# Kernel optimization log

Hardware: AMD Instinct MI355X
Metric: run time of the kernel (lower is better)

Reference implementation:

```python
import jax, jax.numpy as jnp
import numpy as np

BATCH, SEQ, D_MODEL, STATE_DIM = 8, 2048, 1024, 1024


def setup_inputs() -> dict:
    key = jax.random.key(0)
    k1, k2, k3, k4 = jax.random.split(key, 4)
    u = jax.random.normal(k1, (BATCH, SEQ, D_MODEL), dtype=jnp.float32)
    a_params = jax.random.normal(k2, (STATE_DIM // 2,), dtype=jnp.float32) * 0.1
    # nn.Linear default init ~ U(-1/sqrt(fan_in), 1/sqrt(fan_in)); scaled normal is fine for a baseline
    B_w = jax.random.normal(k3, (STATE_DIM, D_MODEL), dtype=jnp.float32) / np.sqrt(D_MODEL).astype(np.float32)
    C_w = jax.random.normal(k4, (D_MODEL, STATE_DIM), dtype=jnp.float32) / np.sqrt(STATE_DIM).astype(np.float32)
    D = jnp.zeros((D_MODEL,), dtype=jnp.float32)
    return {"u": u, "a_params": a_params, "B_w": B_w, "C_w": C_w, "D": D}


def _cayley_circulant_eigenvalues(a_params, n):
    # Build skew-circulant first column: a[0]=0, a[1:n/2]=a_params[:n/2-1], a[n/2]=0,
    # a[n/2+1:] = -flip(a_params[:n/2-1]); eigenvalues are purely imaginary: i*omega.
    half_n = n // 2
    a_full = jnp.zeros((n,), dtype=a_params.dtype)
    a_full = a_full.at[1:half_n].set(a_params[: half_n - 1])
    a_full = a_full.at[half_n + 1 :].set(-a_params[: half_n - 1][::-1])
    omega = jnp.fft.fft(a_full).imag
    # Cayley transform (1 - i*w)/(1 + i*w) = ((1-w^2) - 2iw) / (1+w^2)
    w2 = omega * omega
    denom = 1.0 + w2
    return (((1.0 - w2) / denom) + 1j * (-2.0 * omega / denom)).astype(jnp.complex64)


def reference(u, a_params, B_w, C_w, D):
    n = B_w.shape[0]
    lambdas = _cayley_circulant_eigenvalues(a_params, n)  # (n,) complex64
    Bu = jnp.einsum("bsd,nd->bsn", u, B_w)  # (b, s, n)

    def step(h, bu_t):
        # W h via FFT diagonalization of the circulant W (W real => real part exact)
        Wh = jnp.fft.ifft(lambdas * jnp.fft.fft(h.astype(jnp.float32))).real.astype(h.dtype)
        h_new = Wh + bu_t
        return h_new, h_new

    h0 = jnp.zeros((u.shape[0], n), dtype=u.dtype)
    _, hs = jax.lax.scan(step, h0, jnp.swapaxes(Bu, 0, 1))  # hs: (s, b, n)
    y = jnp.einsum("sbn,dn->bsd", hs, C_w) + D * u  # (b, s, d)
    return y
```

## Files before the change

### kernel.cpp

```cpp
#include <hip/hip_runtime.h>
#include <math.h>

#define BATCH   8
#define SEQLEN  2048
#define DMODEL  1024
#define KFREQ   513
#define NSPEC   1024
#define NPAIR   512
#define BT_ROWS (BATCH*SEQLEN)
#define NC      32
#define TC      64

static_assert(NC * TC == SEQLEN, "chunking must cover SEQLEN");

typedef __attribute__((ext_vector_type(4))) float f32x4;
typedef __attribute__((ext_vector_type(8))) short bf16x8;
typedef unsigned short ushort_t;
typedef unsigned int uint_t;

__device__ __forceinline__ ushort_t f2bf(float f) {
    union { float f; unsigned u; } v; v.f = f;
    unsigned r = v.u + 0x7FFFu + ((v.u >> 16) & 1u);
    return (ushort_t)(r >> 16);
}
__device__ __forceinline__ float bf2f(ushort_t b) {
    union { unsigned u; float f; } v; v.u = ((unsigned)b) << 16;
    return v.f;
}

__device__ __forceinline__ void async_cp16(const void* g, void* l) {
    __builtin_amdgcn_global_load_lds(
        (const __attribute__((address_space(1))) void*)g,
        (__attribute__((address_space(3))) void*)l, 16, 0, 0);
}

#define BAR()   __builtin_amdgcn_s_barrier()
#define PRIO1() __builtin_amdgcn_s_setprio(1)
#define PRIO0() __builtin_amdgcn_s_setprio(0)
#define LGKM0() asm volatile("s_waitcnt lgkmcnt(0)" ::: "memory")
#define LGKM8() asm volatile("s_waitcnt lgkmcnt(8)" ::: "memory")
#define VM6()   asm volatile("s_waitcnt vmcnt(6)" ::: "memory")
#define VM0()   asm volatile("s_waitcnt vmcnt(0)" ::: "memory")

__global__ __launch_bounds__(1024) void compute_lambda(const float* __restrict__ p,
                                                       float* __restrict__ lam,
                                                       const float* __restrict__ Dv,
                                                       int* __restrict__ dflag) {
    __shared__ float stab[1024];
    __shared__ int anyd;
    const int tid = threadIdx.x;
    if (tid == 0) anyd = 0;
    stab[tid] = sinf((float)tid * (6.28318530717958647692f / 1024.0f));
    __syncthreads();
    if (Dv[tid] != 0.0f) anyd = 1;
    if (tid < KFREQ) {
        float om = 0.0f;
        for (int j = 1; j <= 511; ++j)
            om = fmaf(p[j - 1], stab[(j * tid) & 1023], om);
        om *= -2.0f;
        const float w2 = om * om;
        const float den = 1.0f + w2;
        const float re = (1.0f - w2) / den;
        const float im = -2.0f * om / den;
        if (tid == 0)        lam[0] = re;
        else if (tid == 512) lam[1] = re;
        else { lam[2 * tid] = re; lam[2 * tid + 1] = im; }
    }
    __syncthreads();
    if (tid == 0) *dflag = anyd;
}

#define NB_T  (NSPEC * DMODEL / 8 / 256)
#define NB_TR 256
#define NB_U  (BT_ROWS * DMODEL / 8 / 256)
#define NB_CW (DMODEL * DMODEL / 8 / 256)

__global__ __launch_bounds__(256) void prep_all(const float* __restrict__ u,
                                                ushort_t* __restrict__ ub,
                                                const float* __restrict__ Cw,
                                                ushort_t* __restrict__ Cwb,
                                                const float* __restrict__ Bw,
                                                ushort_t* __restrict__ BwTb,
                                                ushort_t* __restrict__ T1b,
                                                ushort_t* __restrict__ T2b) {
    const int bid = blockIdx.x;
    if (bid < 2 * NB_T) {
        __shared__ float stab[1024];
        for (int j = threadIdx.x; j < 1024; j += 256)
            stab[j] = sinf((float)j * (6.28318530717958647692f / 1024.0f));
        __syncthreads();
        const int mode = bid >= NB_T;
        ushort_t* T = mode ? T2b : T1b;
        const int i = (bid - mode * NB_T) * 256 + threadIdx.x;
        const int row = i >> 7;
        const int nb  = (i & 127) << 3;
        const int kf  = (row == 1) ? 512 : (row >> 1);
        const bool sb = (row & 1) && (row != 1);
        float scale = 1.0f;
        if (mode) scale = ((row < 2) ? 1.0f : 2.0f) / 1024.0f;
        ushort_t o[8];
        int m = (kf * nb) & 1023;
#pragma unroll
        for (int j = 0; j < 8; ++j) {
            const float v = sb ? -stab[m] : stab[(m + 256) & 1023];
            o[j] = f2bf(v * scale);
            m = (m + kf) & 1023;
        }
        reinterpret_cast<bf16x8*>(T)[i] = *reinterpret_cast<bf16x8*>(o);
    } else if (bid < 2 * NB_T + NB_TR) {
        __shared__ float tile[64][65];
        const int b2 = bid - 2 * NB_T;
        const int bx = (b2 & 15) * 64;
        const int by = (b2 >> 4) * 64;
        const int lx = threadIdx.x & 63;
        const int ly = threadIdx.x >> 6;
#pragma unroll
        for (int i = 0; i < 16; ++i) {
            const int r = ly + i * 4;
            tile[r][lx] = Bw[(size_t)(by + r) * DMODEL + bx + lx];
        }
        __syncthreads();
#pragma unroll
        for (int i = 0; i < 16; ++i) {
            const int r = ly + i * 4;
            BwTb[(size_t)(bx + r) * DMODEL + by + lx] = f2bf(tile[lx][r]);
        }
    } else {
        const int b3 = bid - (2 * NB_T + NB_TR);
        const float* s; ushort_t* d; int i;
        if (b3 < NB_U) { s = u;  d = ub;  i = b3 * 256 + threadIdx.x; }
        else           { s = Cw; d = Cwb; i = (b3 - NB_U) * 256 + threadIdx.x; }
        const float4 a = reinterpret_cast<const float4*>(s)[2 * i];
        const float4 b = reinterpret_cast<const float4*>(s)[2 * i + 1];
        ushort_t o[8] = {f2bf(a.x), f2bf(a.y), f2bf(a.z), f2bf(a.w),
                         f2bf(b.x), f2bf(b.y), f2bf(b.z), f2bf(b.w)};
        reinterpret_cast<bf16x8*>(d)[i] = *reinterpret_cast<bf16x8*>(o);
    }
}

__global__ __launch_bounds__(256) void gemm128z(const ushort_t* __restrict__ A0,
                                                const ushort_t* __restrict__ B0,
                                                ushort_t* __restrict__ C0,
                                                const ushort_t* __restrict__ A1,
                                                const ushort_t* __restrict__ B1,
                                                ushort_t* __restrict__ C1) {
    const int K = 1024, N = 1024;
    const ushort_t* A = blockIdx.z ? A1 : A0;
    const ushort_t* B = blockIdx.z ? B1 : B0;
    ushort_t*       C = blockIdx.z ? C1 : C0;
    __shared__ ushort_t As[128 * 32];
    __shared__ ushort_t Bs[128 * 32];
    const int tid  = threadIdx.x;
    const int lane = tid & 63;
    const int w    = tid >> 6;
    const int m0 = blockIdx.x * 128;
    const int n0 = blockIdx.y * 128;
    const int wr = (w >> 1) * 64;
    const int wc = (w & 1) * 64;

    f32x4 acc[4][4] = {};

    const int pos  = w * 512 + lane * 8;
    const int srow = pos >> 5;
    const int scol = pos & 31;
    const int lr = lane & 15;
    const int lk = (lane >> 4) * 8;

    for (int k0 = 0; k0 < K; k0 += 32) {
        __syncthreads();
        async_cp16(A + (size_t)(m0 + srow)      * K + k0 + scol, As + w * 512);
        async_cp16(A + (size_t)(m0 + srow + 64) * K + k0 + scol, As + 2048 + w * 512);
        async_cp16(B + (size_t)(n0 + srow)      * K + k0 + scol, Bs + w * 512);
        async_cp16(B + (size_t)(n0 + srow + 64) * K + k0 + scol, Bs + 2048 + w * 512);
        __syncthreads();

        bf16x8 fa[4], fb[4];
#pragma unroll
        for (int mi = 0; mi < 4; ++mi)
            fa[mi] = *reinterpret_cast<const bf16x8*>(&As[(wr + mi * 16 + lr) * 32 + lk]);
#pragma unroll
        for (int ni = 0; ni < 4; ++ni)
            fb[ni] = *reinterpret_cast<const bf16x8*>(&Bs[(wc + ni * 16 + lr) * 32 + lk]);
#pragma unroll
        for (int mi = 0; mi < 4; ++mi)
#pragma unroll
            for (int ni = 0; ni < 4; ++ni)
                acc[mi][ni] = __builtin_amdgcn_mfma_f32_16x16x32_bf16(
                    fa[mi], fb[ni], acc[mi][ni], 0, 0, 0);
    }

    const int rbase = (lane >> 4) * 4;
#pragma unroll
    for (int mi = 0; mi < 4; ++mi)
#pragma unroll
        for (int ni = 0; ni < 4; ++ni) {
            const int col = n0 + wc + ni * 16 + lr;
#pragma unroll
            for (int j = 0; j < 4; ++j) {
                const int row = m0 + wr + mi * 16 + rbase + j;
                C[(size_t)row * N + col] = f2bf(acc[mi][ni][j]);
            }
        }
}

__device__ __forceinline__ void pair_coef(const float* lam, int j,
                                          float& lr, float& lr2, float& cr) {
    const float a = lam[2 * j];
    const float b = lam[2 * j + 1];
    if (j == 0) { lr = a; lr2 = b; cr = 0.0f; }
    else        { lr = a; lr2 = a; cr = b; }
}

template <int MH, int NH>
__device__ __forceinline__ void quad_mfma(f32x4 (&acc)[2][2][4][2],
                                          const bf16x8 (&fa)[4][2],
                                          const bf16x8 (&fb)[2][2]) {
#pragma unroll
    for (int mi = 0; mi < 4; ++mi)
#pragma unroll
        for (int ni = 0; ni < 2; ++ni) {
            acc[MH][NH][mi][ni] = __builtin_amdgcn_mfma_f32_16x16x32_bf16(
                fa[mi][0], fb[ni][0], acc[MH][NH][mi][ni], 0, 0, 0);
            acc[MH][NH][mi][ni] = __builtin_amdgcn_mfma_f32_16x16x32_bf16(
                fa[mi][1], fb[ni][1], acc[MH][NH][mi][ni], 0, 0, 0);
        }
}

__device__ __forceinline__ void ld_fa(bf16x8 (&fa)[4][2], const ushort_t* hb,
                                      int wm, int lr, int c0, int c1) {
#pragma unroll
    for (int mi = 0; mi < 4; ++mi) {
        const ushort_t* p = hb + (wm * 64 + mi * 16 + lr) * 64;
        fa[mi][0] = *reinterpret_cast<const bf16x8*>(p + c0);
        fa[mi][1] = *reinterpret_cast<const bf16x8*>(p + c1);
    }
}
__device__ __forceinline__ void ld_fb(bf16x8 (&fb)[2][2], const ushort_t* hb,
                                      int wn, int lr, int c0, int c1) {
#pragma unroll
    for (int ni = 0; ni < 2; ++ni) {
        const ushort_t* p = hb + (wn * 32 + ni * 16 + lr) * 64;
        fb[ni][0] = *reinterpret_cast<const bf16x8*>(p + c0);
        fb[ni][1] = *reinterpret_cast<const bf16x8*>(p + c1);
    }
}

#define HS_STRIDE 260

template <bool SCANEPI>
__global__ __launch_bounds__(512, 2) void gemm256(const ushort_t* __restrict__ A,
                                                  const ushort_t* __restrict__ B,
                                                  void* __restrict__ Cv,
                                                  int M, int K,
                                                  const float* __restrict__ uu,
                                                  const float* __restrict__ Dv,
                                                  const int* __restrict__ dflag,
                                                  const float* __restrict__ lam,
                                                  float2* __restrict__ G) {
    __shared__ ushort_t smem[66560];
    const int tid  = threadIdx.x;
    const int lane = tid & 63;
    const int w    = tid >> 6;
    const int wm   = w >> 2;
    const int wn   = w & 3;
    const int m0 = blockIdx.x * 256;
    const int n0 = blockIdx.y * 256;
    const int lr = lane & 15;
    const int lk = (lane >> 4) * 8;
    const int xv = (lr & 7) << 3;
    const int c0 = lk ^ xv;
    const int c1 = (32 + lk) ^ xv;

    const int rA = tid >> 3;
    const int cS = ((tid & 7) << 3) ^ ((rA & 7) << 3);
    const int ldsOff = w << 9;

    auto ApH = [&](int buf, int half) { return smem + (buf * 2 + half) * 8192; };
    auto BpH = [&](int buf, int half) { return smem + 32768 + (buf * 2 + half) * 8192; };

    f32x4 acc[2][2][4][2] = {};
    bf16x8 fa[4][2], fbl[2][2], fbh[2][2];

    auto stA = [&](int buf, int half, int k) {
#pragma unroll
        for (int li = 0; li < 2; ++li)
            async_cp16(A + (size_t)(m0 + half * 128 + li * 64 + rA) * K + k + cS,
                       ApH(buf, half) + li * 4096 + ldsOff);
    };
    auto stB = [&](int buf, int half, int k) {
#pragma unroll
        for (int li = 0; li < 2; ++li)
            async_cp16(B + (size_t)(n0 + half * 128 + li * 64 + rA) * K + k + cS,
                       BpH(buf, half) + li * 4096 + ldsOff);
    };

    stA(0, 0, 0); stB(0, 0, 0); stB(0, 1, 0); stA(0, 1, 0);
    stA(1, 0, 64); stB(1, 0, 64); stB(1, 1, 64);
    VM6();
    BAR();

    const int niter = K >> 7;
#pragma unroll 1
    for (int t = 0; t < niter - 1; ++t) {
        const int kb1 = (t << 7) + 64;
        const int kn  = (t + 1) << 7;
        const int kn2 = kn + 64;
        ld_fa(fa, ApH(0, 0), wm, lr, c0, c1);
        ld_fb(fbl, BpH(0, 0), wn, lr, c0, c1);
        stA(1, 1, kb1);
        LGKM8();
        BAR(); LGKM0();
        PRIO1(); quad_mfma<0, 0>(acc, fa, fbl); PRIO0();
        BAR();
        ld_fb(fbh, BpH(0, 1), wn, lr, c0, c1);
        stA(0, 0, kn);
        BAR(); LGKM0();
        PRIO1(); quad_mfma<0, 1>(acc, fa, fbh); PRIO0();
        BAR();
        ld_fa(fa, ApH(0, 1), wm, lr, c0, c1);
        stB(0, 0, kn);
        BAR(); LGKM0();
        PRIO1(); quad_mfma<1, 1>(acc, fa, fbh); PRIO0();
        BAR();
        stB(0, 1, kn);
        VM6();
        BAR();
        PRIO1(); quad_mfma<1, 0>(acc, fa, fbl); PRIO0();
        BAR();
        ld_fa(fa, ApH(1, 0), wm, lr, c0, c1);
        ld_fb(fbl, BpH(1, 0), wn, lr, c0, c1);
        stA(0, 1, kn);
        LGKM8();
        BAR(); LGKM0();
        PRIO1(); quad_mfma<0, 0>(acc, fa, fbl); PRIO0();
        BAR();
        ld_fb(fbh, BpH(1, 1), wn, lr, c0, c1);
        stA(1, 0, kn2);
        BAR(); LGKM0();
        PRIO1(); quad_mfma<0, 1>(acc, fa, fbh); PRIO0();
        BAR();
        ld_fa(fa, ApH(1, 1), wm, lr, c0, c1);
        stB(1, 0, kn2);
        BAR(); LGKM0();
        PRIO1(); quad_mfma<1, 1>(acc, fa, fbh); PRIO0();
        BAR();
        stB(1, 1, kn2);
        VM6();
        BAR();
        PRIO1(); quad_mfma<1, 0>(acc, fa, fbl); PRIO0();
        BAR();
    }
    {
        const int kb1 = ((niter - 1) << 7) + 64;
        ld_fa(fa, ApH(0, 0), wm, lr, c0, c1);
        ld_fb(fbl, BpH(0, 0), wn, lr, c0, c1);
        stA(1, 1, kb1);
        LGKM8();
        BAR(); LGKM0();
        PRIO1(); quad_mfma<0, 0>(acc, fa, fbl); PRIO0();
        BAR();
        ld_fb(fbh, BpH(0, 1), wn, lr, c0, c1);
        BAR(); LGKM0();
        PRIO1(); quad_mfma<0, 1>(acc, fa, fbh); PRIO0();
        BAR();
        ld_fa(fa, ApH(0, 1), wm, lr, c0, c1);
        BAR(); LGKM0();
        PRIO1(); quad_mfma<1, 1>(acc, fa, fbh); PRIO0();
        BAR();
        VM0();
        BAR();
        PRIO1(); quad_mfma<1, 0>(acc, fa, fbl); PRIO0();
        BAR();
        ld_fa(fa, ApH(1, 0), wm, lr, c0, c1);
        ld_fb(fbl, BpH(1, 0), wn, lr, c0, c1);
        BAR(); LGKM0();
        PRIO1(); quad_mfma<0, 0>(acc, fa, fbl); PRIO0();
        BAR();
        ld_fb(fbh, BpH(1, 1), wn, lr, c0, c1);
        BAR(); LGKM0();
        PRIO1(); quad_mfma<0, 1>(acc, fa, fbh); PRIO0();
        BAR();
        ld_fa(fa, ApH(1, 1), wm, lr, c0, c1);
        BAR(); LGKM0();
        PRIO1(); quad_mfma<1, 1>(acc, fa, fbh); PRIO0();
        BAR();
        PRIO1(); quad_mfma<1, 0>(acc, fa, fbl); PRIO0();
    }

    const int rbase = (lane >> 4) * 4;
    if (SCANEPI) {
        BAR();
#pragma unroll
        for (int mh = 0; mh < 2; ++mh)
#pragma unroll
            for (int nh = 0; nh < 2; ++nh)
#pragma unroll
                for (int mi = 0; mi < 4; ++mi)
#pragma unroll
                    for (int ni = 0; ni < 2; ++ni) {
                        const int cl = nh * 128 + wn * 32 + ni * 16 + lr;
#pragma unroll
                        for (int j = 0; j < 4; ++j) {
                            const int rl = mh * 128 + wm * 64 + mi * 16 + rbase + j;
                            smem[rl * HS_STRIDE + cl] = f2bf(acc[mh][nh][mi][ni][j]);
                        }
                    }
        BAR();
        const int chunk = tid >> 7;
        const int p = tid & 127;
        const int jg = (n0 >> 1) + p;
        float lr_, lr2_, cr_;
        pair_coef(lam, jg, lr_, lr2_, cr_);
        uint_t* gout = reinterpret_cast<uint_t*>((ushort_t*)Cv +
                        (size_t)(m0 + chunk * TC) * NSPEC) + jg;
        float er = 0.0f, ei = 0.0f;
        for (int t = 0; t < TC; ++t) {
            const uint_t v = *reinterpret_cast<const uint_t*>(
                &smem[(chunk * TC + t) * HS_STRIDE + 2 * p]);
            const float ur = bf2f((ushort_t)(v & 0xFFFF));
            const float ui = bf2f((ushort_t)(v >> 16));
            const float nr = fmaf(lr_, er, fmaf(-cr_, ei, ur));
            const float ni = fmaf(lr2_, ei, fmaf(cr_, er, ui));
            gout[(size_t)t * NPAIR] = (uint_t)f2bf(nr) | ((uint_t)f2bf(ni) << 16);
            er = nr; ei = ni;
        }
        const int b = m0 >> 11;
        const int cg = ((m0 & 2047) >> 6) + chunk;
        G[(size_t)(b * NC + cg) * NPAIR + jg] = make_float2(er, ei);
    } else {
        float* C = (float*)Cv;
        const bool du = (*dflag != 0);
#pragma unroll
        for (int mh = 0; mh < 2; ++mh)
#pragma unroll
            for (int nh = 0; nh < 2; ++nh)
#pragma unroll
                for (int mi = 0; mi < 4; ++mi)
#pragma unroll
                    for (int ni = 0; ni < 2; ++ni) {
                        const int col = n0 + nh * 128 + wn * 32 + ni * 16 + lr;
#pragma unroll
                        for (int j = 0; j < 4; ++j) {
                            const int row = m0 + mh * 128 + wm * 64 + mi * 16 + rbase + j;
                            float v = acc[mh][nh][mi][ni][j];
                            if (du) v = fmaf(Dv[col], uu[(size_t)row * DMODEL + col], v);
                            C[(size_t)row * DMODEL + col] = v;
                        }
                    }
    }
}

__global__ __launch_bounds__(256) void scan_carry(const float2* __restrict__ G,
                                                  const float* __restrict__ lam,
                                                  float2* __restrict__ Ac) {
    const int gid = blockIdx.x * 256 + threadIdx.x;
    if (gid >= BATCH * NPAIR) return;
    const int j = gid & (NPAIR - 1);
    const int b = gid >> 9;
    float lr, lr2, cr;
    pair_coef(lam, j, lr, lr2, cr);
    float pr = lr, pr2 = lr2, pc = cr;
    for (int s = 0; s < 6; ++s) {
        const float nr  = pr * pr - pc * pc;
        const float nr2 = pr2 * pr2 - pc * pc;
        const float npc = pc * (pr + pr2);
        pr = nr; pr2 = nr2; pc = npc;
    }
    float er = 0.0f, ei = 0.0f;
    for (int c = 0; c < NC; ++c) {
        const int idx = (b * NC + c) * NPAIR + j;
        Ac[idx] = make_float2(er, ei);
        const float2 g = G[idx];
        const float nr = fmaf(pr, er, fmaf(-pc, ei, g.x));
        const float ni = fmaf(pr2, ei, fmaf(pc, er, g.y));
        er = nr; ei = ni;
    }
}

__global__ __launch_bounds__(256) void scan_applyc(ushort_t* __restrict__ UHb,
                                                   const float* __restrict__ lam,
                                                   const float2* __restrict__ Ac) {
    const int gid = blockIdx.x * 256 + threadIdx.x;
    const int j = gid & (NPAIR - 1);
    const int c = (gid >> 9) & (NC - 1);
    const int b = gid >> 14;
    if (c == 0) return;
    float lr, lr2, cr;
    pair_coef(lam, j, lr, lr2, cr);
    const float2 e = Ac[(b * NC + c) * NPAIR + j];
    float sr = fmaf(lr, e.x, -cr * e.y);
    float si = fmaf(lr2, e.y, cr * e.x);
    uint_t* base = reinterpret_cast<uint_t*>(
        UHb + (size_t)(b * SEQLEN + c * TC) * NSPEC) + j;
    for (int t = 0; t < TC; ++t) {
        const uint_t v = base[(size_t)t * NPAIR];
        const float hr = bf2f((ushort_t)(v & 0xFFFF)) + sr;
        const float hi = bf2f((ushort_t)(v >> 16)) + si;
        base[(size_t)t * NPAIR] = (uint_t)f2bf(hr) | ((uint_t)f2bf(hi) << 16);
        const float nsr = fmaf(lr, sr, -cr * si);
        const float nsi = fmaf(lr2, si, cr * sr);
        sr = nsr; si = nsi;
    }
}

extern "C" void kernel_launch(void* const* d_in, const int* in_sizes, int n_in,
                              void* d_out, int out_size, void* d_ws, size_t ws_size,
                              hipStream_t stream) {
    const float* u  = (const float*)d_in[0];
    const float* ap = (const float*)d_in[1];
    const float* Bw = (const float*)d_in[2];
    const float* Cw = (const float*)d_in[3];
    const float* Dv = (const float*)d_in[4];
    float* out = (float*)d_out;

    char* ws = (char*)d_ws;
    size_t off = 0;
    auto carve = [&](size_t bytes) { char* p = ws + off; off += (bytes + 255) & ~(size_t)255; return p; };

    ushort_t* UHb  = (ushort_t*)carve((size_t)BT_ROWS * NSPEC * sizeof(ushort_t));
    ushort_t* ub   = (ushort_t*)carve((size_t)BT_ROWS * DMODEL * sizeof(ushort_t));
    ushort_t* T1b  = (ushort_t*)carve((size_t)NSPEC * DMODEL * sizeof(ushort_t));
    ushort_t* T2b  = (ushort_t*)carve((size_t)NSPEC * DMODEL * sizeof(ushort_t));
    ushort_t* BwTb = (ushort_t*)carve((size_t)DMODEL * DMODEL * sizeof(ushort_t));
    ushort_t* Cwb  = (ushort_t*)carve((size_t)DMODEL * DMODEL * sizeof(ushort_t));
    ushort_t* W1b  = (ushort_t*)carve((size_t)NSPEC * DMODEL * sizeof(ushort_t));
    ushort_t* W2b  = (ushort_t*)carve((size_t)DMODEL * NSPEC * sizeof(ushort_t));
    float*    lam  = (float*)   carve(NSPEC * sizeof(float));
    int*      dflag= (int*)     carve(sizeof(int));
    float2*   G    = (float2*)  carve((size_t)BATCH * NC * NPAIR * sizeof(float2));
    float2*   Ac   = (float2*)  carve((size_t)BATCH * NC * NPAIR * sizeof(float2));

    compute_lambda<<<1, 1024, 0, stream>>>(ap, lam, Dv, dflag);

    prep_all<<<2 * NB_T + NB_TR + NB_U + NB_CW, 256, 0, stream>>>(
        u, ub, Cw, Cwb, Bw, BwTb, T1b, T2b);

    {
        dim3 g(8, 8, 2);
        gemm128z<<<g, 256, 0, stream>>>(T1b, BwTb, W1b, Cwb, T2b, W2b);
    }

    {
        dim3 g(BT_ROWS / 256, NSPEC / 256);
        gemm256<true><<<g, 512, 0, stream>>>(ub, W1b, UHb,
            BT_ROWS, DMODEL, nullptr, nullptr, dflag, lam, G);
    }

    scan_carry<<<(BATCH * NPAIR + 255) / 256, 256, 0, stream>>>(G, lam, Ac);
    scan_applyc<<<BATCH * NC * NPAIR / 256, 256, 0, stream>>>(UHb, lam, Ac);

    {
        dim3 g(BT_ROWS / 256, DMODEL / 256);
        gemm256<false><<<g, 512, 0, stream>>>(UHb, W2b, out,
            BT_ROWS, NSPEC, u, Dv, dflag, lam, nullptr);
    }
}
```

Before: 149.0 us.

## Merge small prep kernels and fold carry scan into apply kernel

```diff
diff --git a/kernel.cpp b/kernel.cpp
--- a/kernel.cpp
+++ b/kernel.cpp
@@ -42,41 +42,17 @@
 #define VM6()   asm volatile("s_waitcnt vmcnt(6)" ::: "memory")
 #define VM0()   asm volatile("s_waitcnt vmcnt(0)" ::: "memory")
 
-__global__ __launch_bounds__(1024) void compute_lambda(const float* __restrict__ p,
-                                                       float* __restrict__ lam,
-                                                       const float* __restrict__ Dv,
-                                                       int* __restrict__ dflag) {
-    __shared__ float stab[1024];
-    __shared__ int anyd;
-    const int tid = threadIdx.x;
-    if (tid == 0) anyd = 0;
-    stab[tid] = sinf((float)tid * (6.28318530717958647692f / 1024.0f));
-    __syncthreads();
-    if (Dv[tid] != 0.0f) anyd = 1;
-    if (tid < KFREQ) {
-        float om = 0.0f;
-        for (int j = 1; j <= 511; ++j)
-            om = fmaf(p[j - 1], stab[(j * tid) & 1023], om);
-        om *= -2.0f;
-        const float w2 = om * om;
-        const float den = 1.0f + w2;
-        const float re = (1.0f - w2) / den;
-        const float im = -2.0f * om / den;
-        if (tid == 0)        lam[0] = re;
-        else if (tid == 512) lam[1] = re;
-        else { lam[2 * tid] = re; lam[2 * tid + 1] = im; }
-    }
-    __syncthreads();
-    if (tid == 0) *dflag = anyd;
-}
+#define SINSTEP 0.00613592315154256491887f
 
 #define NB_T  (NSPEC * DMODEL / 8 / 256)
 #define NB_TR 256
+#define NB_CW (DMODEL * DMODEL / 8 / 256)
 #define NB_U  (BT_ROWS * DMODEL / 8 / 256)
-#define NB_CW (DMODEL * DMODEL / 8 / 256)
-
-__global__ __launch_bounds__(256) void prep_all(const float* __restrict__ u,
-                                                ushort_t* __restrict__ ub,
+
+__global__ __launch_bounds__(256) void prep_all(const float* __restrict__ ap,
+                                                float* __restrict__ lam,
+                                                const float* __restrict__ Dv,
+                                                int* __restrict__ dflag,
                                                 const float* __restrict__ Cw,
                                                 ushort_t* __restrict__ Cwb,
                                                 const float* __restrict__ Bw,
@@ -84,14 +60,39 @@
                                                 ushort_t* __restrict__ T1b,
                                                 ushort_t* __restrict__ T2b) {
     const int bid = blockIdx.x;
-    if (bid < 2 * NB_T) {
+    if (bid == 0) {
+        __shared__ float stab[1024];
+        __shared__ int anyd;
+        if (threadIdx.x == 0) anyd = 0;
+        for (int j = threadIdx.x; j < 1024; j += 256)
+            stab[j] = sinf((float)j * SINSTEP);
+        __syncthreads();
+        for (int q = threadIdx.x; q < 1024; q += 256)
+            if (Dv[q] != 0.0f) anyd = 1;
+        for (int f = threadIdx.x; f < KFREQ; f += 256) {
+            float om = 0.0f;
+            for (int j = 1; j <= 511; ++j)
+                om = fmaf(ap[j - 1], stab[(j * f) & 1023], om);
+            om *= -2.0f;
+            const float w2 = om * om;
+            const float den = 1.0f + w2;
+            const float re = (1.0f - w2) / den;
+            const float im = -2.0f * om / den;
+            if (f == 0)        lam[0] = re;
+            else if (f == 512) lam[1] = re;
+            else { lam[2 * f] = re; lam[2 * f + 1] = im; }
+        }
+        __syncthreads();
+        if (threadIdx.x == 0) *dflag = anyd;
+    } else if (bid < 1 + 2 * NB_T) {
         __shared__ float stab[1024];
         for (int j = threadIdx.x; j < 1024; j += 256)
-            stab[j] = sinf((float)j * (6.28318530717958647692f / 1024.0f));
+            stab[j] = sinf((float)j * SINSTEP);
         __syncthreads();
-        const int mode = bid >= NB_T;
+        const int t = bid - 1;
+        const int mode = t >= NB_T;
         ushort_t* T = mode ? T2b : T1b;
-        const int i = (bid - mode * NB_T) * 256 + threadIdx.x;
+        const int i = (t - mode * NB_T) * 256 + threadIdx.x;
         const int row = i >> 7;
         const int nb  = (i & 127) << 3;
         const int kf  = (row == 1) ? 512 : (row >> 1);
@@ -107,9 +108,9 @@
             m = (m + kf) & 1023;
         }
         reinterpret_cast<bf16x8*>(T)[i] = *reinterpret_cast<bf16x8*>(o);
-    } else if (bid < 2 * NB_T + NB_TR) {
+    } else if (bid < 1 + 2 * NB_T + NB_TR) {
         __shared__ float tile[64][65];
-        const int b2 = bid - 2 * NB_T;
+        const int b2 = bid - (1 + 2 * NB_T);
         const int bx = (b2 & 15) * 64;
         const int by = (b2 >> 4) * 64;
         const int lx = threadIdx.x & 63;
@@ -126,35 +127,45 @@
             BwTb[(size_t)(bx + r) * DMODEL + by + lx] = f2bf(tile[lx][r]);
         }
     } else {
-        const int b3 = bid - (2 * NB_T + NB_TR);
-        const float* s; ushort_t* d; int i;
-        if (b3 < NB_U) { s = u;  d = ub;  i = b3 * 256 + threadIdx.x; }
-        else           { s = Cw; d = Cwb; i = (b3 - NB_U) * 256 + threadIdx.x; }
-        const float4 a = reinterpret_cast<const float4*>(s)[2 * i];
-        const float4 b = reinterpret_cast<const float4*>(s)[2 * i + 1];
+        const int b3 = bid - (1 + 2 * NB_T + NB_TR);
+        const int i = b3 * 256 + threadIdx.x;
+        const float4 a = reinterpret_cast<const float4*>(Cw)[2 * i];
+        const float4 b = reinterpret_cast<const float4*>(Cw)[2 * i + 1];
         ushort_t o[8] = {f2bf(a.x), f2bf(a.y), f2bf(a.z), f2bf(a.w),
                          f2bf(b.x), f2bf(b.y), f2bf(b.z), f2bf(b.w)};
-        reinterpret_cast<bf16x8*>(d)[i] = *reinterpret_cast<bf16x8*>(o);
-    }
-}
-
-__global__ __launch_bounds__(256) void gemm128z(const ushort_t* __restrict__ A0,
-                                                const ushort_t* __restrict__ B0,
-                                                ushort_t* __restrict__ C0,
-                                                const ushort_t* __restrict__ A1,
-                                                const ushort_t* __restrict__ B1,
-                                                ushort_t* __restrict__ C1) {
+        reinterpret_cast<bf16x8*>(Cwb)[i] = *reinterpret_cast<bf16x8*>(o);
+    }
+}
+
+__global__ __launch_bounds__(256) void conv_and_gemm128(
+        const float* __restrict__ u, ushort_t* __restrict__ ub,
+        const ushort_t* __restrict__ A0, const ushort_t* __restrict__ B0,
+        ushort_t* __restrict__ C0,
+        const ushort_t* __restrict__ A1, const ushort_t* __restrict__ B1,
+        ushort_t* __restrict__ C1) {
+    const int bid = blockIdx.x;
+    if (bid >= 128) {
+        const int i = (bid - 128) * 256 + threadIdx.x;
+        const float4 a = reinterpret_cast<const float4*>(u)[2 * i];
+        const float4 b = reinterpret_cast<const float4*>(u)[2 * i + 1];
+        ushort_t o[8] = {f2bf(a.x), f2bf(a.y), f2bf(a.z), f2bf(a.w),
+                         f2bf(b.x), f2bf(b.y), f2bf(b.z), f2bf(b.w)};
+        reinterpret_cast<bf16x8*>(ub)[i] = *reinterpret_cast<bf16x8*>(o);
+        return;
+    }
     const int K = 1024, N = 1024;
-    const ushort_t* A = blockIdx.z ? A1 : A0;
-    const ushort_t* B = blockIdx.z ? B1 : B0;
-    ushort_t*       C = blockIdx.z ? C1 : C0;
+    const int z = bid >> 6;
+    const ushort_t* A = z ? A1 : A0;
+    const ushort_t* B = z ? B1 : B0;
+    ushort_t*       C = z ? C1 : C0;
+    const int g = bid & 63;
+    const int m0 = (g >> 3) * 128;
+    const int n0 = (g & 7) * 128;
     __shared__ ushort_t As[128 * 32];
     __shared__ ushort_t Bs[128 * 32];
     const int tid  = threadIdx.x;
     const int lane = tid & 63;
     const int w    = tid >> 6;
-    const int m0 = blockIdx.x * 128;
-    const int n0 = blockIdx.y * 128;
     const int wr = (w >> 1) * 64;
     const int wc = (w & 1) * 64;
 
@@ -450,13 +461,14 @@
     }
 }
 
-__global__ __launch_bounds__(256) void scan_carry(const float2* __restrict__ G,
-                                                  const float* __restrict__ lam,
-                                                  float2* __restrict__ Ac) {
+__global__ __launch_bounds__(256) void scan_applyc(ushort_t* __restrict__ UHb,
+                                                   const float* __restrict__ lam,
+                                                   const float2* __restrict__ G) {
     const int gid = blockIdx.x * 256 + threadIdx.x;
-    if (gid >= BATCH * NPAIR) return;
     const int j = gid & (NPAIR - 1);
-    const int b = gid >> 9;
+    const int s9 = gid >> 9;
+    const int c = 1 + s9 % 31;
+    const int b = s9 / 31;
     float lr, lr2, cr;
     pair_coef(lam, j, lr, lr2, cr);
     float pr = lr, pr2 = lr2, pc = cr;
@@ -467,29 +479,14 @@
         pr = nr; pr2 = nr2; pc = npc;
     }
     float er = 0.0f, ei = 0.0f;
-    for (int c = 0; c < NC; ++c) {
-        const int idx = (b * NC + c) * NPAIR + j;
-        Ac[idx] = make_float2(er, ei);
-        const float2 g = G[idx];
+    for (int cp = 0; cp < c; ++cp) {
+        const float2 g = G[(size_t)(b * NC + cp) * NPAIR + j];
         const float nr = fmaf(pr, er, fmaf(-pc, ei, g.x));
         const float ni = fmaf(pr2, ei, fmaf(pc, er, g.y));
         er = nr; ei = ni;
     }
-}
-
-__global__ __launch_bounds__(256) void scan_applyc(ushort_t* __restrict__ UHb,
-                                                   const float* __restrict__ lam,
-                                                   const float2* __restrict__ Ac) {
-    const int gid = blockIdx.x * 256 + threadIdx.x;
-    const int j = gid & (NPAIR - 1);
-    const int c = (gid >> 9) & (NC - 1);
-    const int b = gid >> 14;
-    if (c == 0) return;
-    float lr, lr2, cr;
-    pair_coef(lam, j, lr, lr2, cr);
-    const float2 e = Ac[(b * NC + c) * NPAIR + j];
-    float sr = fmaf(lr, e.x, -cr * e.y);
-    float si = fmaf(lr2, e.y, cr * e.x);
+    float sr = fmaf(lr, er, -cr * ei);
+    float si = fmaf(lr2, ei, cr * er);
     uint_t* base = reinterpret_cast<uint_t*>(
         UHb + (size_t)(b * SEQLEN + c * TC) * NSPEC) + j;
     for (int t = 0; t < TC; ++t) {
@@ -528,17 +525,12 @@
     float*    lam  = (float*)   carve(NSPEC * sizeof(float));
     int*      dflag= (int*)     carve(sizeof(int));
     float2*   G    = (float2*)  carve((size_t)BATCH * NC * NPAIR * sizeof(float2));
-    float2*   Ac   = (float2*)  carve((size_t)BATCH * NC * NPAIR * sizeof(float2));
-
-    compute_lambda<<<1, 1024, 0, stream>>>(ap, lam, Dv, dflag);
-
-    prep_all<<<2 * NB_T + NB_TR + NB_U + NB_CW, 256, 0, stream>>>(
-        u, ub, Cw, Cwb, Bw, BwTb, T1b, T2b);
-
-    {
-        dim3 g(8, 8, 2);
-        gemm128z<<<g, 256, 0, stream>>>(T1b, BwTb, W1b, Cwb, T2b, W2b);
-    }
+
+    prep_all<<<1 + 2 * NB_T + NB_TR + NB_CW, 256, 0, stream>>>(
+        ap, lam, Dv, dflag, Cw, Cwb, Bw, BwTb, T1b, T2b);
+
+    conv_and_gemm128<<<128 + NB_U, 256, 0, stream>>>(
+        u, ub, T1b, BwTb, W1b, Cwb, T2b, W2b);
 
     {
         dim3 g(BT_ROWS / 256, NSPEC / 256);
@@ -546,8 +538,7 @@
             BT_ROWS, DMODEL, nullptr, nullptr, dflag, lam, G);
     }
 
-    scan_carry<<<(BATCH * NPAIR + 255) / 256, 256, 0, stream>>>(G, lam, Ac);
-    scan_applyc<<<BATCH * NC * NPAIR / 256, 256, 0, stream>>>(UHb, lam, Ac);
+    scan_applyc<<<BATCH * 31 * NPAIR / 256, 256, 0, stream>>>(UHb, lam, G);
 
     {
         dim3 g(BT_ROWS / 256, DMODEL / 256);
```

Result: slower. 163.1 us (+9.4%).
